# Kernel tuning notes

Hardware: AMD Instinct MI355X
Metric: run time of the kernel (lower is better)

Reference implementation:

```python
import jax, jax.numpy as jnp
import numpy as np

B, G, N_IN, N_HID, N_OUT = 2, 4096, 8, 32, 32
ALPHA, BETA, BN_EPS = 0.005, 5e-5, 1e-5
EDGE_P = 0.05  # adjacency density


def _lin_init(k, fan_in, fan_out):
    k1, k2 = jax.random.split(k)
    lim = 1.0 / np.sqrt(fan_in)
    W = jax.random.uniform(k1, (fan_in, fan_out), minval=-lim, maxval=lim, dtype=jnp.float32)
    b = jax.random.uniform(k2, (fan_out,), minval=-lim, maxval=lim, dtype=jnp.float32)
    return W, b


def setup_inputs() -> dict:
    key = jax.random.key(0)
    ks = jax.random.split(key, 12)
    W_infer, b_infer = _lin_init(ks[0], N_IN, N_HID)
    W_e1, b_e1 = _lin_init(ks[1], 2 * N_HID, 1)
    W_e2, b_e2 = _lin_init(ks[2], 2 * N_HID, 1)
    W_n1, b_n1 = _lin_init(ks[3], 2 * N_HID, N_OUT)
    W_n2, b_n2 = _lin_init(ks[4], 2 * N_HID, N_OUT)
    W_m1, b_m1 = _lin_init(ks[5], 2 * N_HID, N_OUT)
    W_m2, b_m2 = _lin_init(ks[6], 2 * N_HID, N_OUT)
    x = jax.random.normal(ks[7], (B, G, N_IN), dtype=jnp.float32)
    edges1 = jax.random.bernoulli(ks[8], EDGE_P, (G, G)).astype(jnp.float32)
    edges2 = jax.random.bernoulli(ks[9], EDGE_P, (G, G)).astype(jnp.float32)
    bn_gamma = jnp.ones((G,), jnp.float32)
    bn_beta = jnp.zeros((G,), jnp.float32)
    return dict(x=x, edges1=edges1, edges2=edges2, W_infer=W_infer, b_infer=b_infer,
                W_e1=W_e1, b_e1=b_e1, W_e2=W_e2, b_e2=b_e2,
                W_n1=W_n1, b_n1=b_n1, W_n2=W_n2, b_n2=b_n2,
                W_m1=W_m1, b_m1=b_m1, W_m2=W_m2, b_m2=b_m2,
                bn_gamma=bn_gamma, bn_beta=bn_beta)


def _mp_block(x, adj, coef, W_e, b_e, W_n, b_n, W_m, b_m):
    # x: [B,G,H]. Torch builds edge feature at flat index k=i*G+j as cat([x_j, x_i])
    # (shape2 = col gather, shape1 = row gather). We keep the same math without
    # materializing the [B,G*G,2H] tensor.
    Hh = x.shape[-1]
    s_src = x @ W_e[:Hh]   # [B,G,1]  (x_j part of mlp_edge)
    s_dst = x @ W_e[Hh:]   # [B,G,1]  (x_i part of mlp_edge)
    logits = s_dst[:, :, None, 0] + s_src[:, None, :, 0] + b_e[0]   # [B,G,G] at (i,j)
    w = adj + coef * (adj == 0).astype(x.dtype)                     # ori_edge + coef*thres_edge
    e = jax.nn.sigmoid(logits) * w[None]                            # [B,G,G]
    # receive at node i: sum_j e_ij * [x_j, x_i]
    recv_src = jnp.einsum('bij,bjh->bih', e, x)                     # sum_j e_ij x_j
    recv_dst = x * jnp.sum(e, axis=2)[..., None]                    # x_i * sum_j e_ij
    recv = jnp.concatenate([recv_src, recv_dst], axis=-1)           # [B,G,2H]
    recv = jax.nn.elu(recv @ W_n + b_n)                             # nodes_mlp + elu
    upd = jnp.concatenate([recv, x], axis=-1) @ W_m + b_m           # mesg_merge (mode='cat')
    return jax.nn.elu(upd)


def _forward(x, edges1, edges2, W_infer, b_infer, W_e1, b_e1, W_e2, b_e2,
             W_n1, b_n1, W_n2, b_n2, W_m1, b_m1, W_m2, b_m2, bn_gamma, bn_beta):
    h = jax.nn.elu(x @ W_infer + b_infer)                           # infer + elu, [B,G,H]
    h = _mp_block(h, edges1, ALPHA, W_e1, b_e1, W_n1, b_n1, W_m1, b_m1)
    # BatchNorm1d(gene_num) on [B, G, n_out]: per-gene stats over (batch, feature)
    mu = jnp.mean(h, axis=(0, 2), keepdims=True)
    var = jnp.var(h, axis=(0, 2), keepdims=True)
    h = (h - mu) * jax.lax.rsqrt(var + BN_EPS)
    h = h * bn_gamma[None, :, None] + bn_beta[None, :, None]
    return _mp_block(h, edges2, BETA, W_e2, b_e2, W_n2, b_n2, W_m2, b_m2)


def reference(x, edges1, edges2, W_infer, b_infer, W_e1, b_e1, W_e2, b_e2,
              W_n1, b_n1, W_n2, b_n2, W_m1, b_m1, W_m2, b_m2, bn_gamma, bn_beta):
    return _forward(x, edges1, edges2, W_infer, b_infer, W_e1, b_e1, W_e2, b_e2,
                    W_n1, b_n1, W_n2, b_n2, W_m1, b_m1, W_m2, b_m2, bn_gamma, bn_beta)
```

## Files before the change

### kernel.cpp

```cpp
#include <hip/hip_runtime.h>

#define G 4096
#define BSZ 2
#define NIN 8
#define HID 32
#define NLOG2E (-1.4426950408889634f)

typedef __attribute__((ext_vector_type(8))) short short8;
typedef __attribute__((ext_vector_type(4))) float floatx4;
typedef unsigned short ushort_t;
typedef unsigned int uint_t;
typedef unsigned long long u64_t;

__device__ __forceinline__ float elu1(float v) {
    return v > 0.f ? v : (__expf(v) - 1.f);
}
__device__ __forceinline__ ushort_t f2bf(float f) {
    unsigned u = __float_as_uint(f);
    u += 0x7fffu + ((u >> 16) & 1u);
    return (ushort_t)(u >> 16);
}

__global__ __launch_bounds__(256) void k_pack(
    const float* __restrict__ e1, const float* __restrict__ e2,
    uint_t* __restrict__ pk) {
    int wid = blockIdx.x * 4 + (threadIdx.x >> 6);
    int lane = threadIdx.x & 63;
    int matrix = wid >> 11;
    int ul = (wid & 2047) * 128;
    const float* src = matrix ? e2 : e1;
    u64_t* dst = (u64_t*)(pk + (size_t)matrix * 524288);
    for (int s = 0; s < 128; s += 8) {
        float v[8];
#pragma unroll
        for (int k = 0; k < 8; k++)
            v[k] = src[(size_t)(ul + s + k) * 64 + lane];
        u64_t mk[8];
#pragma unroll
        for (int k = 0; k < 8; k++) mk[k] = __ballot(v[k] != 0.f);
        if (lane == 0) {
#pragma unroll
            for (int k = 0; k < 8; k++) dst[ul + s + k] = mk[k];
        }
    }
}

__global__ __launch_bounds__(256) void k_setup1(
    const float* __restrict__ x, const float* __restrict__ W,
    const float* __restrict__ bias, const float* __restrict__ We,
    float* __restrict__ h0, ushort_t* __restrict__ hTb,
    float* __restrict__ ssrc, float* __restrict__ sdst) {
    __shared__ __align__(16) ushort_t hs[HID][264];
    int tid = threadIdx.x;
    int t = blockIdx.x * 256 + tid;
    int b = t >> 12;
    int g0 = (blockIdx.x & 15) * 256;
    float xin[NIN];
    const float* xp = x + t * NIN;
#pragma unroll
    for (int k = 0; k < NIN; k++) xin[k] = xp[k];
    float ss = 0.f, sd = 0.f;
    float* hp = h0 + (size_t)t * HID;
#pragma unroll
    for (int o = 0; o < HID; o++) {
        float v = bias[o];
#pragma unroll
        for (int k = 0; k < NIN; k++) v += xin[k] * W[k * HID + o];
        v = elu1(v);
        hp[o] = v;
        hs[o][tid] = f2bf(v);
        ss += v * We[o];
        sd += v * We[HID + o];
    }
    ssrc[t] = ss;
    sdst[t] = sd;
    __syncthreads();
#pragma unroll
    for (int p = 0; p < 4; p++) {
        int row = p * 8 + (tid >> 5);
        int c = (tid & 31) * 8;
        short8 v8 = *(const short8*)&hs[row][c];
        *(short8*)(void*)&hTb[(size_t)(b * HID + row) * G + g0 + c] = v8;
    }
}

template <bool DO_BN>
__global__ __launch_bounds__(512, 2) void k_fused(
    const uint_t* __restrict__ pk, const float* __restrict__ ssrc,
    const float* __restrict__ sdst, const ushort_t* __restrict__ hTb_in,
    const float* __restrict__ bep, float coef, const float* __restrict__ hin,
    const float* __restrict__ Wn, const float* __restrict__ bnb,
    const float* __restrict__ Wm, const float* __restrict__ bmb,
    const float* __restrict__ gamma, const float* __restrict__ beta,
    const float* __restrict__ We2, float* __restrict__ outp,
    ushort_t* __restrict__ hTb_out, float* __restrict__ s2s,
    float* __restrict__ s2d) {
    union SMemU {
        float ssm[BSZ][G];
        struct {
            float rec[32][68];
            float rec2[32][68];
            float esg[16][2];
            ushort_t tb[BSZ][HID][16];
        } p;
    };
    __shared__ __align__(16) SMemU sm;
    __shared__ __align__(16) uint_t abits[128][16];
    __shared__ __align__(16) float red[6][64][9];
    __shared__ __align__(16) float Wns[2048];
    __shared__ __align__(16) float Wms[2048];

    int tid = threadIdx.x;
    int g0 = blockIdx.x * 16;

    ((float4*)Wns)[tid] = ((const float4*)Wn)[tid];
    ((float4*)Wms)[tid] = ((const float4*)Wm)[tid];
#pragma unroll
    for (int r = 0; r < 4; r++) {
        int idx = r * 2048 + tid * 4;
        int bb = idx >> 12, j = idx & 4095;
        float4 s4 = *(const float4*)&ssrc[bb * G + j];
        s4.x *= NLOG2E; s4.y *= NLOG2E; s4.z *= NLOG2E; s4.w *= NLOG2E;
        *(float4*)&sm.ssm[bb][j] = s4;
    }
    {
        int ms = tid >> 5, d0 = (tid & 31) * 4;
        uint4 pv = *(const uint4*)&pk[(size_t)(g0 + ms) * 128 + d0];
        abits[d0 + 0][ms] = pv.x;
        abits[d0 + 1][ms] = pv.y;
        abits[d0 + 2][ms] = pv.z;
        abits[d0 + 3][ms] = pv.w;
    }

    int l = tid & 63, w = tid >> 6;
    int jq = w >> 1, b = w & 1;
    int m = l & 15, kg = l >> 4;
    float sd2 = (sdst[b * G + g0 + m] + bep[0]) * NLOG2E;
    float wm1 = 1.f - coef;
    int jstart = jq * 1024;
    const ushort_t* hb0 = hTb_in + (size_t)(b * HID + m) * G + jstart + kg * 8;
    const ushort_t* hb1 = hb0 + (size_t)16 * G;
    floatx4 c0 = {0.f, 0.f, 0.f, 0.f}, c1 = {0.f, 0.f, 0.f, 0.f};
    float es = 0.f;
    short8 pb0[2], pb1[2];
#pragma unroll
    for (int d = 0; d < 2; d++) {
        pb0[d] = *(const short8*)(const void*)(hb0 + d * 32);
        pb1[d] = *(const short8*)(const void*)(hb1 + d * 32);
    }
    __syncthreads();
    const float* svp = &sm.ssm[b][jstart + kg * 8];
    const uint_t* abp = &abits[jq * 32][m];

#pragma unroll 4
    for (int jc = 0; jc < 32; jc++) {
        int cur = jc & 1;
        short8 bf0 = pb0[cur], bf1 = pb1[cur];
        if (jc + 2 < 32) {
            int o = (jc + 2) * 32;
            pb0[cur] = *(const short8*)(const void*)(hb0 + o);
            pb1[cur] = *(const short8*)(const void*)(hb1 + o);
        }
        uint_t bw = abp[jc * 16];
        float4 s0 = *(const float4*)&svp[jc * 32];
        float4 s1 = *(const float4*)&svp[jc * 32 + 4];
        float sv[8] = {s0.x, s0.y, s0.z, s0.w, s1.x, s1.y, s1.z, s1.w};
        short8 af;
#pragma unroll
        for (int t = 0; t < 8; t++) {
            float bitf = (float)((bw >> (kg * 8 + t)) & 1u);
            float wgt = __builtin_fmaf(bitf, wm1, coef);
            float ex = exp2f(sd2 + sv[t]);
            float e = __builtin_amdgcn_rcpf(1.f + ex) * wgt;
            es += e;
            af[t] = (short)f2bf(e);
        }
        c0 = __builtin_amdgcn_mfma_f32_16x16x32_bf16(af, bf0, c0, 0, 0, 0);
        c1 = __builtin_amdgcn_mfma_f32_16x16x32_bf16(af, bf1, c1, 0, 0, 0);
    }
    if (jq) {
        int widx = (jq - 1) * 2 + b;
#pragma unroll
        for (int r = 0; r < 4; r++) {
            red[widx][l][r] = c0[r];
            red[widx][l][4 + r] = c1[r];
        }
        red[widx][l][8] = es;
    }
    __syncthreads();
    if (!jq) {
#pragma unroll
        for (int q = 0; q < 3; q++) {
            int widx = q * 2 + b;
#pragma unroll
            for (int r = 0; r < 4; r++) {
                c0[r] += red[widx][l][r];
                c1[r] += red[widx][l][4 + r];
            }
            es += red[widx][l][8];
        }
        es += __shfl_xor(es, 16);
        es += __shfl_xor(es, 32);
#pragma unroll
        for (int r = 0; r < 4; r++) {
            int gene = (l >> 4) * 4 + r;
            sm.p.rec[gene * 2 + b][m] = c0[r];
            sm.p.rec[gene * 2 + b][16 + m] = c1[r];
        }
        if (l < 16) sm.p.esg[l][b] = es;
    }
    __syncthreads();

    int rl = tid >> 5, hh = tid & 31;
#pragma unroll
    for (int rp = 0; rp < 2; rp++) {
        int row = rp * 16 + rl;
        int gene = row >> 1, bb = row & 1;
        float xv = hin[((size_t)(bb * G + g0 + gene)) * HID + hh];
        sm.p.rec[row][32 + hh] = xv * sm.p.esg[gene][bb];
    }
    __syncthreads();

#pragma unroll
    for (int rp = 0; rp < 2; rp++) {
        int row = rp * 16 + rl;
        int gene = row >> 1, bb = row & 1;
        float v = bnb[hh];
#pragma unroll
        for (int k4 = 0; k4 < 16; k4++) {
            float4 r4 = *(const float4*)&sm.p.rec[row][k4 * 4];
            v += r4.x * Wns[(k4 * 4 + 0) * HID + hh];
            v += r4.y * Wns[(k4 * 4 + 1) * HID + hh];
            v += r4.z * Wns[(k4 * 4 + 2) * HID + hh];
            v += r4.w * Wns[(k4 * 4 + 3) * HID + hh];
        }
        v = elu1(v);
        float xv = hin[((size_t)(bb * G + g0 + gene)) * HID + hh];
        sm.p.rec2[row][hh] = v;
        sm.p.rec2[row][32 + hh] = xv;
        float u = bmb[hh];
#pragma unroll
        for (int k4 = 0; k4 < 16; k4++) {
            float4 r4 = *(const float4*)&sm.p.rec2[row][k4 * 4];
            u += r4.x * Wms[(k4 * 4 + 0) * HID + hh];
            u += r4.y * Wms[(k4 * 4 + 1) * HID + hh];
            u += r4.z * Wms[(k4 * 4 + 2) * HID + hh];
            u += r4.w * Wms[(k4 * 4 + 3) * HID + hh];
        }
        float h1v = elu1(u);
        if (!DO_BN) {
            outp[((size_t)(bb * G + g0 + gene)) * HID + hh] = h1v;
        } else {
            float s = h1v, sq = h1v * h1v;
#pragma unroll
            for (int mm = 32; mm; mm >>= 1) {
                s += __shfl_xor(s, mm);
                sq += __shfl_xor(sq, mm);
            }
            float mu = s * (1.f / 64.f);
            float var = sq * (1.f / 64.f) - mu * mu;
            float rstd = rsqrtf(var + 1e-5f);
            float hn = (h1v - mu) * rstd * gamma[g0 + gene] + beta[g0 + gene];
            outp[((size_t)(bb * G + g0 + gene)) * HID + hh] = hn;
            sm.p.tb[bb][hh][gene] = f2bf(hn);
            float ps = hn * We2[hh], pd = hn * We2[HID + hh];
#pragma unroll
            for (int mm = 16; mm; mm >>= 1) {
                ps += __shfl_xor(ps, mm);
                pd += __shfl_xor(pd, mm);
            }
            if (hh == 0) {
                s2s[bb * G + g0 + gene] = ps;
                s2d[bb * G + g0 + gene] = pd;
            }
        }
    }
    if (DO_BN) {
        __syncthreads();
        if (tid < 128) {
            int b2 = tid >> 6, c = (tid >> 1) & 31, half = tid & 1;
            short8 v8 = *(const short8*)&sm.p.tb[b2][c][half * 8];
            *(short8*)(void*)&hTb_out[(size_t)(b2 * HID + c) * G + g0 + half * 8] = v8;
        }
    }
}

extern "C" void kernel_launch(void* const* d_in, const int* in_sizes, int n_in,
                              void* d_out, int out_size, void* d_ws, size_t ws_size,
                              hipStream_t stream) {
    const float* x      = (const float*)d_in[0];
    const float* edges1 = (const float*)d_in[1];
    const float* edges2 = (const float*)d_in[2];
    const float* W_inf  = (const float*)d_in[3];
    const float* b_inf  = (const float*)d_in[4];
    const float* W_e1   = (const float*)d_in[5];
    const float* b_e1   = (const float*)d_in[6];
    const float* W_e2   = (const float*)d_in[7];
    const float* b_e2   = (const float*)d_in[8];
    const float* W_n1   = (const float*)d_in[9];
    const float* b_n1   = (const float*)d_in[10];
    const float* W_n2   = (const float*)d_in[11];
    const float* b_n2   = (const float*)d_in[12];
    const float* W_m1   = (const float*)d_in[13];
    const float* b_m1   = (const float*)d_in[14];
    const float* W_m2   = (const float*)d_in[15];
    const float* b_m2   = (const float*)d_in[16];
    const float* bn_g   = (const float*)d_in[17];
    const float* bn_b   = (const float*)d_in[18];
    float* out = (float*)d_out;

    float* ws = (float*)d_ws;
    float* h0   = ws;
    float* h1n  = ws + 262144;
    float* s1s  = ws + 524288;
    float* s1d  = ws + 532480;
    float* s2s  = ws + 540672;
    float* s2d  = ws + 548864;
    ushort_t* hTb  = (ushort_t*)(ws + 557056);
    ushort_t* hTb2 = (ushort_t*)(ws + 688128);
    uint_t* pk = (uint_t*)(ws + 819200);

    const float ALPHA = 0.005f, BETA = 5e-5f;

    k_pack<<<1024, 256, 0, stream>>>(edges1, edges2, pk);
    k_setup1<<<32, 256, 0, stream>>>(x, W_inf, b_inf, W_e1, h0, hTb, s1s, s1d);
    k_fused<true><<<G / 16, 512, 0, stream>>>(
        pk, s1s, s1d, hTb, b_e1, ALPHA, h0, W_n1, b_n1, W_m1, b_m1,
        bn_g, bn_b, W_e2, h1n, hTb2, s2s, s2d);
    k_fused<false><<<G / 16, 512, 0, stream>>>(
        pk + 524288, s2s, s2d, hTb2, b_e2, BETA, h1n, W_n2, b_n2, W_m2, b_m2,
        nullptr, nullptr, nullptr, out, nullptr, nullptr, nullptr);
}
```

Baseline: 242.4 us.

## Fuse adjacency bit-packing into the fused message-passing kernels

Drops the separate k_pack kernel. Each k_fused block now reads its 16 rows of the float adjacency matrix directly and builds the bitmask in shared memory, using nibble packing plus xor shuffles. This removes one kernel launch and the write and re-read of the packed mask. In exchange, each fused kernel prologue now streams 256KB of adjacency per block before its main loop, which may leave it latency-bound.

```diff
diff --git a/kernel.cpp b/kernel.cpp
--- a/kernel.cpp
+++ b/kernel.cpp
@@ -10,7 +10,6 @@
 typedef __attribute__((ext_vector_type(4))) float floatx4;
 typedef unsigned short ushort_t;
 typedef unsigned int uint_t;
-typedef unsigned long long u64_t;
 
 __device__ __forceinline__ float elu1(float v) {
     return v > 0.f ? v : (__expf(v) - 1.f);
@@ -19,30 +18,6 @@
     unsigned u = __float_as_uint(f);
     u += 0x7fffu + ((u >> 16) & 1u);
     return (ushort_t)(u >> 16);
-}
-
-__global__ __launch_bounds__(256) void k_pack(
-    const float* __restrict__ e1, const float* __restrict__ e2,
-    uint_t* __restrict__ pk) {
-    int wid = blockIdx.x * 4 + (threadIdx.x >> 6);
-    int lane = threadIdx.x & 63;
-    int matrix = wid >> 11;
-    int ul = (wid & 2047) * 128;
-    const float* src = matrix ? e2 : e1;
-    u64_t* dst = (u64_t*)(pk + (size_t)matrix * 524288);
-    for (int s = 0; s < 128; s += 8) {
-        float v[8];
-#pragma unroll
-        for (int k = 0; k < 8; k++)
-            v[k] = src[(size_t)(ul + s + k) * 64 + lane];
-        u64_t mk[8];
-#pragma unroll
-        for (int k = 0; k < 8; k++) mk[k] = __ballot(v[k] != 0.f);
-        if (lane == 0) {
-#pragma unroll
-            for (int k = 0; k < 8; k++) dst[ul + s + k] = mk[k];
-        }
-    }
 }
 
 __global__ __launch_bounds__(256) void k_setup1(
@@ -86,7 +61,7 @@
 
 template <bool DO_BN>
 __global__ __launch_bounds__(512, 2) void k_fused(
-    const uint_t* __restrict__ pk, const float* __restrict__ ssrc,
+    const float* __restrict__ adj, const float* __restrict__ ssrc,
     const float* __restrict__ sdst, const ushort_t* __restrict__ hTb_in,
     const float* __restrict__ bep, float coef, const float* __restrict__ hin,
     const float* __restrict__ Wn, const float* __restrict__ bnb,
@@ -112,6 +87,7 @@
 
     int tid = threadIdx.x;
     int g0 = blockIdx.x * 16;
+    int l = tid & 63, w = tid >> 6;
 
     ((float4*)Wns)[tid] = ((const float4*)Wn)[tid];
     ((float4*)Wms)[tid] = ((const float4*)Wm)[tid];
@@ -123,16 +99,23 @@
         s4.x *= NLOG2E; s4.y *= NLOG2E; s4.z *= NLOG2E; s4.w *= NLOG2E;
         *(float4*)&sm.ssm[bb][j] = s4;
     }
-    {
-        int ms = tid >> 5, d0 = (tid & 31) * 4;
-        uint4 pv = *(const uint4*)&pk[(size_t)(g0 + ms) * 128 + d0];
-        abits[d0 + 0][ms] = pv.x;
-        abits[d0 + 1][ms] = pv.y;
-        abits[d0 + 2][ms] = pv.z;
-        abits[d0 + 3][ms] = pv.w;
-    }
-
-    int l = tid & 63, w = tid >> 6;
+#pragma unroll
+    for (int rr = 0; rr < 2; rr++) {
+        int row = 2 * w + rr;
+        const float* ar = adj + (size_t)(g0 + row) * G;
+#pragma unroll
+        for (int it = 0; it < 16; it++) {
+            float4 v4 = *(const float4*)&ar[it * 256 + l * 4];
+            uint_t nib = (uint_t)(v4.x != 0.f) | ((uint_t)(v4.y != 0.f) << 1) |
+                         ((uint_t)(v4.z != 0.f) << 2) | ((uint_t)(v4.w != 0.f) << 3);
+            uint_t wd = nib << ((l & 7) * 4);
+            wd |= __shfl_xor(wd, 1);
+            wd |= __shfl_xor(wd, 2);
+            wd |= __shfl_xor(wd, 4);
+            if ((l & 7) == 0) abits[it * 8 + (l >> 3)][row] = wd;
+        }
+    }
+
     int jq = w >> 1, b = w & 1;
     int m = l & 15, kg = l >> 4;
     float sd2 = (sdst[b * G + g0 + m] + bep[0]) * NLOG2E;
@@ -318,16 +301,14 @@
     float* s2d  = ws + 548864;
     ushort_t* hTb  = (ushort_t*)(ws + 557056);
     ushort_t* hTb2 = (ushort_t*)(ws + 688128);
-    uint_t* pk = (uint_t*)(ws + 819200);
 
     const float ALPHA = 0.005f, BETA = 5e-5f;
 
-    k_pack<<<1024, 256, 0, stream>>>(edges1, edges2, pk);
     k_setup1<<<32, 256, 0, stream>>>(x, W_inf, b_inf, W_e1, h0, hTb, s1s, s1d);
     k_fused<true><<<G / 16, 512, 0, stream>>>(
-        pk, s1s, s1d, hTb, b_e1, ALPHA, h0, W_n1, b_n1, W_m1, b_m1,
+        edges1, s1s, s1d, hTb, b_e1, ALPHA, h0, W_n1, b_n1, W_m1, b_m1,
         bn_g, bn_b, W_e2, h1n, hTb2, s2s, s2d);
     k_fused<false><<<G / 16, 512, 0, stream>>>(
-        pk + 524288, s2s, s2d, hTb2, b_e2, BETA, h1n, W_n2, b_n2, W_m2, b_m2,
+        edges2, s2s, s2d, hTb2, b_e2, BETA, h1n, W_n2, b_n2, W_m2, b_m2,
         nullptr, nullptr, nullptr, out, nullptr, nullptr, nullptr);
 }
```

Measured after the change: 248.2 us. 2.4% more time.
